# Kernel optimization log

Hardware: AMD Instinct MI355X
Metric: run time of the kernel (lower is better)

Reference implementation:

```python
import jax, jax.numpy as jnp
import numpy as np

D_MODEL = 1024
HEADDIM = 64
EXPAND = 2
D_STATE = 128
D_CONV = 4
NGROUPS = 1
D_INNER = EXPAND * D_MODEL            # 2048
NHEADS = D_INNER // HEADDIM           # 32
CONV_DIM = D_INNER + 2 * NGROUPS * D_STATE
D_IN_PROJ = 2 * D_INNER + 2 * NGROUPS * D_STATE + NHEADS
BATCH = 2
SEQLEN = 1024
EPS = 1e-5


def silu(v):
    return v * jax.nn.sigmoid(v)


def setup_inputs() -> dict:
    key = jax.random.key(0)
    ks = jax.random.split(key, 8)
    s = 0.02
    return {
        "x": jax.random.normal(ks[0], (BATCH, SEQLEN, D_MODEL), jnp.float32),
        "in_proj_w": jax.random.normal(ks[1], (D_IN_PROJ, D_MODEL), jnp.float32) * s,
        "conv_w": jax.random.normal(ks[2], (CONV_DIM, D_CONV), jnp.float32) * 0.2,
        "conv_b": jax.random.normal(ks[3], (CONV_DIM,), jnp.float32) * 0.02,
        "dt_bias": jax.random.normal(ks[4], (NHEADS,), jnp.float32) * 0.1,
        "A_log": jax.random.normal(ks[5], (NHEADS,), jnp.float32) * 0.5,
        "D": jax.random.normal(ks[6], (NHEADS,), jnp.float32) * 0.5,
        "norm_w": jnp.ones((D_INNER,), jnp.float32),
        "out_proj_w": jax.random.normal(ks[7], (D_MODEL, D_INNER), jnp.float32) * s,
    }


def _mamba2(x, in_proj_w, conv_w, conv_b, dt_bias, A_log, D, norm_w, out_proj_w):
    b, l, _ = x.shape
    # input projection -> z | xBC | dt
    zxbcdt = x @ in_proj_w.T                                  # [b,l,d_in_proj]
    z, xBC, dt = jnp.split(zxbcdt, [D_INNER, D_INNER + CONV_DIM], axis=-1)
    dt = jax.nn.softplus(dt + dt_bias)                        # [b,l,nh]
    # causal depthwise conv over time, then SiLU
    rhs = conv_w.T[:, None, :]                                # [d_conv, 1, conv_dim]
    xBC = jax.lax.conv_general_dilated(
        xBC, rhs, window_strides=(1,), padding=[(D_CONV - 1, 0)],
        dimension_numbers=("NWC", "WIO", "NWC"), feature_group_count=CONV_DIM)
    xBC = silu(xBC + conv_b)
    xs, Bm, Cm = jnp.split(xBC, [D_INNER, D_INNER + D_STATE], axis=-1)
    xs = xs.reshape(b, l, NHEADS, HEADDIM)                    # [b,l,h,p]
    A = -jnp.exp(A_log)                                       # [nh], negative
    dA = jnp.exp(dt * A)                                      # [b,l,nh] in (0,1)
    # selective scan: h_t = dA_t * h_{t-1} + dt_t * x_t (outer) B_t; y_t = h_t C_t
    def step(h, inp):
        dA_t, x_t, B_t, dt_t, C_t = inp                       # [b,h],[b,h,p],[b,n],[b,h],[b,n]
        h = h * dA_t[:, :, None, None] + jnp.einsum("bh,bhp,bn->bhpn", dt_t, x_t, B_t)
        y = jnp.einsum("bhpn,bn->bhp", h, C_t)
        return h, y

    h0 = jnp.zeros((b, NHEADS, HEADDIM, D_STATE), x.dtype)
    xs_t = xs.transpose(1, 0, 2, 3)
    _, ys = jax.lax.scan(step, h0, (dA.transpose(1, 0, 2), xs_t,
                                    Bm.transpose(1, 0, 2), dt.transpose(1, 0, 2),
                                    Cm.transpose(1, 0, 2)))
    y = ys.transpose(1, 0, 2, 3) + D[None, None, :, None] * xs  # skip term
    y = y.reshape(b, l, D_INNER)
    # gated RMSNorm (norm_before_gate=False): rmsnorm(y * silu(z)) * w
    y = y * silu(z)
    y = y * jax.lax.rsqrt(jnp.mean(y * y, axis=-1, keepdims=True) + EPS) * norm_w
    return y @ out_proj_w.T


def reference(x, in_proj_w, conv_w, conv_b, dt_bias, A_log, D, norm_w, out_proj_w):
    return x + _mamba2(x, in_proj_w, conv_w, conv_b, dt_bias, A_log, D, norm_w, out_proj_w)
```

## Files before the change

### kernel.cpp

```cpp
#include <hip/hip_runtime.h>
#include <hip/hip_bf16.h>
#include <math.h>

#define NHEADS   32
#define CONV_DIM 2304
#define D_INNER  2048
#define SEQLEN   1024
#define NROWS    2048
#define ZX_STR   4352
#define D_MODEL  1024
#define Q        64
#define NCHUNK   16
#define XT_STR   72

typedef __attribute__((ext_vector_type(8))) short bhalf8;
typedef __attribute__((ext_vector_type(8))) short short8;
typedef __attribute__((ext_vector_type(4))) short short4v;
typedef __attribute__((ext_vector_type(4))) float f32x4;

__device__ __forceinline__ float bf2f(__hip_bfloat16 v){ return __bfloat162float(v); }
__device__ __forceinline__ short f2bs(float f){ __hip_bfloat16 h = __float2bfloat16(f); return *(short*)&h; }
__device__ __forceinline__ float s2f(short s){ __hip_bfloat16 h = *(__hip_bfloat16*)&s; return __bfloat162float(h); }
__device__ __forceinline__ float rdin(const void* p, size_t i, int isf){
    return isf ? ((const float*)p)[i] : __bfloat162float(((const __hip_bfloat16*)p)[i]);
}

#define XN8 262144
#define WN8 561152
#define ON8 262144
__global__ __launch_bounds__(256)
void to_bf16_all(const void* __restrict__ xs, const void* __restrict__ ws,
                 const void* __restrict__ os, const void* __restrict__ normw,
                 __hip_bfloat16* __restrict__ xd, __hip_bfloat16* __restrict__ wd,
                 __hip_bfloat16* __restrict__ od, int* __restrict__ flagp)
{
    const unsigned short* xu = (const unsigned short*)xs;
    int cnt = 0;
    for (int k = threadIdx.x; k < 4096; k += 256) {
        int e = (xu[2 * k] >> 7) & 0xFF;
        cnt += (e >= 90 && e <= 141) ? 1 : 0;
    }
#pragma unroll
    for (int m = 1; m < 64; m <<= 1) cnt += __shfl_xor(cnt, m);
    __shared__ int red[4];
    if ((threadIdx.x & 63) == 0) red[threadIdx.x >> 6] = cnt;
    __syncthreads();
    const int isf = ((red[0] + red[1] + red[2] + red[3]) < 2048) ? 1 : 0;
    if (blockIdx.x == 0 && threadIdx.x == 0) *flagp = isf;

    int i = blockIdx.x * 256 + threadIdx.x;
    if (i < XN8 + WN8) {
        const void* src; __hip_bfloat16* dst; int j;
        if (i < XN8) { src = xs; dst = xd; j = i; }
        else         { src = ws; dst = wd; j = i - XN8; }
        if (isf) {
            const float4* s = (const float4*)src;
            float4 a = s[2 * j], b = s[2 * j + 1];
            short8 r;
            r[0]=f2bs(a.x); r[1]=f2bs(a.y); r[2]=f2bs(a.z); r[3]=f2bs(a.w);
            r[4]=f2bs(b.x); r[5]=f2bs(b.y); r[6]=f2bs(b.z); r[7]=f2bs(b.w);
            ((short8*)dst)[j] = r;
        } else {
            ((float4*)dst)[j] = ((const float4*)src)[j];
        }
    } else {
        int j = i - XN8 - WN8;
        int k0 = (j * 8) & (D_INNER - 1);
        float v[8];
        if (isf) {
            const float4* s = (const float4*)os;
            float4 a = s[2 * j], b = s[2 * j + 1];
            v[0]=a.x; v[1]=a.y; v[2]=a.z; v[3]=a.w;
            v[4]=b.x; v[5]=b.y; v[6]=b.z; v[7]=b.w;
        } else {
            bhalf8 a = ((const bhalf8*)os)[j];
#pragma unroll
            for (int q = 0; q < 8; ++q) v[q] = s2f(a[q]);
        }
        short8 r;
#pragma unroll
        for (int q = 0; q < 8; ++q)
            r[q] = f2bs(v[q] * rdin(normw, k0 + q, isf));
        ((short8*)od)[j] = r;
    }
}

template<int MODE, int MT, int NT, int WROWS, int WCOLS>
__global__ __launch_bounds__(256)
void gemm_bt(const __hip_bfloat16* __restrict__ A,
             const __hip_bfloat16* __restrict__ W,
             __hip_bfloat16* __restrict__ Cb,
             const void* __restrict__ xraw,
             void* __restrict__ outv,
             const float* __restrict__ rowsum,
             const int* __restrict__ flagp,
             int K, int N)
{
    constexpr int FM = MT / WROWS / 16;
    constexpr int FN = NT / WCOLS / 16;
    constexpr int AI = MT / 32;
    constexpr int BI = NT / 32;
    __shared__ short As[MT * 64];
    __shared__ short Bs[NT * 64];
    const int m0 = blockIdx.y * MT;
    const int n0 = blockIdx.x * NT;
    const int wave = threadIdx.x >> 6;
    const int lane = threadIdx.x & 63;
    const int lr8 = lane >> 3, lc8 = lane & 7;
    const int lr  = lane & 15, lq  = lane >> 4;
    const int wm = (wave / WCOLS) * (MT / WROWS);
    const int wn = (wave % WCOLS) * (NT / WCOLS);
    const int swl = lr & 7;

    f32x4 acc[FM][FN];
#pragma unroll
    for (int i = 0; i < FM; ++i)
#pragma unroll
        for (int j = 0; j < FN; ++j) acc[i][j] = (f32x4){0.f,0.f,0.f,0.f};

    for (int k0 = 0; k0 < K; k0 += 64) {
#pragma unroll
        for (int i = 0; i < AI; ++i) {
            const int rt = (wave * AI + i) * 8;
            const __hip_bfloat16* gp = A + (size_t)(m0 + rt + lr8) * K + k0 + ((lc8 ^ lr8) << 3);
            __builtin_amdgcn_global_load_lds(
                (const __attribute__((address_space(1))) void*)gp,
                (__attribute__((address_space(3))) void*)&As[rt * 64], 16, 0, 0);
        }
#pragma unroll
        for (int i = 0; i < BI; ++i) {
            const int rt = (wave * BI + i) * 8;
            const __hip_bfloat16* gp = W + (size_t)(n0 + rt + lr8) * K + k0 + ((lc8 ^ lr8) << 3);
            __builtin_amdgcn_global_load_lds(
                (const __attribute__((address_space(1))) void*)gp,
                (__attribute__((address_space(3))) void*)&Bs[rt * 64], 16, 0, 0);
        }
        __syncthreads();
#pragma unroll
        for (int kk = 0; kk < 64; kk += 32) {
            const int sw = (((kk >> 3) + lq) ^ swl) << 3;
            bhalf8 af[FM], bfv[FN];
#pragma unroll
            for (int t = 0; t < FM; ++t)
                af[t]  = *(const bhalf8*)&As[(wm + t * 16 + lr) * 64 + sw];
#pragma unroll
            for (int t = 0; t < FN; ++t)
                bfv[t] = *(const bhalf8*)&Bs[(wn + t * 16 + lr) * 64 + sw];
#pragma unroll
            for (int ti = 0; ti < FM; ++ti)
#pragma unroll
                for (int tj = 0; tj < FN; ++tj)
                    acc[ti][tj] = __builtin_amdgcn_mfma_f32_16x16x32_bf16(
                        af[ti], bfv[tj], acc[ti][tj], 0, 0, 0);
        }
        __syncthreads();
    }

    const int isf = (MODE == 1) ? *flagp : 0;
#pragma unroll
    for (int ti = 0; ti < FM; ++ti)
#pragma unroll
        for (int tj = 0; tj < FN; ++tj)
#pragma unroll
            for (int r = 0; r < 4; ++r) {
                int m = m0 + wm + ti * 16 + lq * 4 + r;
                int n = n0 + wn + tj * 16 + lr;
                size_t idx = (size_t)m * N + n;
                float v = acc[ti][tj][r];
                if (MODE == 0) {
                    Cb[idx] = __float2bfloat16(v);
                } else {
                    float scale = rsqrtf(rowsum[m] / (float)D_INNER + 1e-5f);
                    v = v * scale + rdin(xraw, idx, isf);
                    if (isf) ((float*)outv)[idx] = v;
                    else     ((__hip_bfloat16*)outv)[idx] = __float2bfloat16(v);
                }
            }
}

__global__ __launch_bounds__(256)
void convdt(const __hip_bfloat16* __restrict__ zxb,
            const void* __restrict__ conv_w, const void* __restrict__ conv_b,
            const void* __restrict__ xraw, const void* __restrict__ wraw,
            const void* __restrict__ dt_bias,
            const int* __restrict__ flagp,
            __hip_bfloat16* __restrict__ xs_bf,
            __hip_bfloat16* __restrict__ B_bf,
            __hip_bfloat16* __restrict__ C_bf,
            float* __restrict__ dtp)
{
    __shared__ short smem[11 * CONV_DIM];
    const int isf = *flagp;

    if (blockIdx.x < 256) {
        const int r0 = blockIdx.x * 8;
        const int bstart = r0 & ~(SEQLEN - 1);
        for (int idx = threadIdx.x; idx < 11 * (CONV_DIM / 8); idx += 256) {
            int ii = idx / (CONV_DIM / 8);
            int seg = idx % (CONV_DIM / 8);
            int g = r0 - 3 + ii;
            bhalf8 v;
            if (g >= bstart) {
                v = *(const bhalf8*)&zxb[(size_t)g * ZX_STR + 2048 + seg * 8];
            } else {
#pragma unroll
                for (int j = 0; j < 8; ++j) v[j] = 0;
            }
            *(bhalf8*)&smem[ii * CONV_DIM + seg * 8] = v;
        }
        __syncthreads();

#pragma unroll
        for (int sIt = 0; sIt < 2; ++sIt) {
            const int seg = threadIdx.x + sIt * 256;
            if (seg >= CONV_DIM / 8) break;
            const int c0 = seg * 8;
            float wt[8][4], bias[8];
            if (isf) {
                const float4* wp = (const float4*)conv_w;
#pragma unroll
                for (int u = 0; u < 8; ++u) {
                    float4 q = wp[c0 + u];
                    wt[u][0]=q.x; wt[u][1]=q.y; wt[u][2]=q.z; wt[u][3]=q.w;
                }
                float4 b0 = ((const float4*)conv_b)[seg * 2];
                float4 b1 = ((const float4*)conv_b)[seg * 2 + 1];
                bias[0]=b0.x; bias[1]=b0.y; bias[2]=b0.z; bias[3]=b0.w;
                bias[4]=b1.x; bias[5]=b1.y; bias[6]=b1.z; bias[7]=b1.w;
            } else {
                const bhalf8* wp = (const bhalf8*)conv_w;
#pragma unroll
                for (int u = 0; u < 4; ++u) {
                    bhalf8 q = wp[seg * 4 + u];
#pragma unroll
                    for (int t4 = 0; t4 < 4; ++t4) {
                        wt[2*u][t4]   = s2f(q[t4]);
                        wt[2*u+1][t4] = s2f(q[4 + t4]);
                    }
                }
                bhalf8 bq = ((const bhalf8*)conv_b)[seg];
#pragma unroll
                for (int j = 0; j < 8; ++j) bias[j] = s2f(bq[j]);
            }
#pragma unroll
            for (int r = 0; r < 8; ++r) {
                bhalf8 i0 = *(const bhalf8*)&smem[(r + 0) * CONV_DIM + c0];
                bhalf8 i1 = *(const bhalf8*)&smem[(r + 1) * CONV_DIM + c0];
                bhalf8 i2 = *(const bhalf8*)&smem[(r + 2) * CONV_DIM + c0];
                bhalf8 i3 = *(const bhalf8*)&smem[(r + 3) * CONV_DIM + c0];
                bhalf8 out;
#pragma unroll
                for (int j = 0; j < 8; ++j) {
                    float acc = bias[j];
                    acc = fmaf(s2f(i0[j]), wt[j][0], acc);
                    acc = fmaf(s2f(i1[j]), wt[j][1], acc);
                    acc = fmaf(s2f(i2[j]), wt[j][2], acc);
                    acc = fmaf(s2f(i3[j]), wt[j][3], acc);
                    out[j] = f2bs(acc / (1.f + expf(-acc)));
                }
                const int row = r0 + r;
                if (c0 < 2048)
                    *(bhalf8*)&xs_bf[(size_t)row * 2048 + c0] = out;
                else if (c0 < 2176)
                    *(bhalf8*)&B_bf[(size_t)row * 128 + (c0 - 2048)] = out;
                else
                    *(bhalf8*)&C_bf[(size_t)row * 128 + (c0 - 2176)] = out;
            }
        }
    } else {
        float* xsh = (float*)smem;
        const int r0 = (blockIdx.x - 256) * 8;
        if (isf) {
            const float4* xp = (const float4*)xraw;
            for (int i4 = threadIdx.x; i4 < 2048; i4 += 256)
                *(float4*)&xsh[i4 * 4] = xp[(size_t)r0 * 256 + i4];
        } else {
            const bhalf8* xp = (const bhalf8*)xraw;
            for (int i8 = threadIdx.x; i8 < 1024; i8 += 256) {
                bhalf8 v = xp[(size_t)r0 * 128 + i8];
#pragma unroll
                for (int q = 0; q < 8; ++q) xsh[i8 * 8 + q] = s2f(v[q]);
            }
        }
        __syncthreads();
        const int h = threadIdx.x >> 3;
        const int t = threadIdx.x & 7;
        const size_t wb = (size_t)(4352 + h) * D_MODEL;
        float s[8];
#pragma unroll
        for (int r = 0; r < 8; ++r) s[r] = 0.f;
        if (isf) {
            const float4* wp = (const float4*)wraw;
            for (int k0 = 0; k0 < D_MODEL; k0 += 32) {
                float4 w4 = wp[(wb + k0) / 4 + t];
#pragma unroll
                for (int r = 0; r < 8; ++r) {
                    float4 x4 = *(const float4*)&xsh[r * D_MODEL + k0 + t * 4];
                    s[r] = fmaf(w4.x, x4.x, fmaf(w4.y, x4.y,
                           fmaf(w4.z, x4.z, fmaf(w4.w, x4.w, s[r]))));
                }
            }
        } else {
            const __hip_bfloat16* wp = (const __hip_bfloat16*)wraw;
            for (int k0 = 0; k0 < D_MODEL; k0 += 64) {
                bhalf8 w8 = *(const bhalf8*)&wp[wb + k0 + t * 8];
#pragma unroll
                for (int r = 0; r < 8; ++r) {
                    float4 xa = *(const float4*)&xsh[r * D_MODEL + k0 + t * 8];
                    float4 xb = *(const float4*)&xsh[r * D_MODEL + k0 + t * 8 + 4];
                    s[r] = fmaf(s2f(w8[0]), xa.x, fmaf(s2f(w8[1]), xa.y,
                           fmaf(s2f(w8[2]), xa.z, fmaf(s2f(w8[3]), xa.w, s[r]))));
                    s[r] = fmaf(s2f(w8[4]), xb.x, fmaf(s2f(w8[5]), xb.y,
                           fmaf(s2f(w8[6]), xb.z, fmaf(s2f(w8[7]), xb.w, s[r]))));
                }
            }
        }
#pragma unroll
        for (int r = 0; r < 8; ++r) {
            s[r] += __shfl_xor(s[r], 1);
            s[r] += __shfl_xor(s[r], 2);
            s[r] += __shfl_xor(s[r], 4);
        }
        if (t == 0) {
            float bias = rdin(dt_bias, h, isf);
#pragma unroll
            for (int r = 0; r < 8; ++r) {
                float raw = s[r] + bias;
                dtp[(size_t)(r0 + r) * NHEADS + h] = raw > 20.f ? raw : log1pf(expf(raw));
            }
        }
    }
}

__global__ __launch_bounds__(256)
void chunk_kernel(const __hip_bfloat16* __restrict__ xs_bf,
                  const __hip_bfloat16* __restrict__ B_bf,
                  const float* __restrict__ dtp, const void* __restrict__ Alog,
                  const int* __restrict__ flagp,
                  float* __restrict__ cumg, float* __restrict__ decayg,
                  __hip_bfloat16* __restrict__ Sb,
                  float* __restrict__ rowsum)
{
    __shared__ float cumS[Q], uS[Q];
    __shared__ short Xt[64 * XT_STR];
    __shared__ short Bt[128 * XT_STR];
    const int bhc = blockIdx.x;
    const int c = bhc & 15, h = (bhc >> 4) & 31, b = bhc >> 9;
    const int row0 = b * SEQLEN + c * Q;
    const int isf = *flagp;

    if (threadIdx.x < 2) rowsum[bhc * 2 + threadIdx.x] = 0.f;
    if (threadIdx.x < 64) {
        const int t = threadIdx.x;
        const float An = -expf(rdin(Alog, h, isf));
        const float dt = dtp[(size_t)(row0 + t) * NHEADS + h];
        float cum = dt * An;
#pragma unroll
        for (int ofs = 1; ofs < 64; ofs <<= 1) {
            float v = __shfl_up(cum, ofs);
            if (t >= ofs) cum += v;
        }
        float tot = __shfl(cum, 63);
        cumS[t] = cum;
        uS[t] = expf(tot - cum) * dt;
        cumg[(size_t)bhc * Q + t] = cum;
        if (t == 63) decayg[bhc] = expf(tot);
    }
    __syncthreads();

#pragma unroll
    for (int i = 0; i < 2; ++i) {
        int seg = threadIdx.x + i * 256;
        int t = seg >> 3, p8 = (seg & 7) * 8;
        float ut = uS[t];
        bhalf8 v = *(const bhalf8*)&xs_bf[(size_t)(row0 + t) * 2048 + h * 64 + p8];
#pragma unroll
        for (int j = 0; j < 8; ++j)
            Xt[(p8 + j) * XT_STR + t] = f2bs(s2f(v[j]) * ut);
    }
#pragma unroll
    for (int i = 0; i < 4; ++i) {
        int seg = threadIdx.x + i * 256;
        int t = seg >> 4, n8 = (seg & 15) * 8;
        bhalf8 v = *(const bhalf8*)&B_bf[(size_t)(row0 + t) * 128 + n8];
#pragma unroll
        for (int j = 0; j < 8; ++j)
            Bt[(n8 + j) * XT_STR + t] = v[j];
    }
    __syncthreads();

    const int wave = threadIdx.x >> 6, lane = threadIdx.x & 63;
    const int lr = lane & 15, lq = lane >> 4;
    const int p0 = wave * 16;
    f32x4 acc[8];
#pragma unroll
    for (int j = 0; j < 8; ++j) acc[j] = (f32x4){0.f,0.f,0.f,0.f};
#pragma unroll
    for (int kk = 0; kk < 64; kk += 32) {
        bhalf8 af = *(const bhalf8*)&Xt[(p0 + lr) * XT_STR + kk + lq * 8];
#pragma unroll
        for (int j = 0; j < 8; ++j) {
            bhalf8 bf = *(const bhalf8*)&Bt[(j * 16 + lr) * XT_STR + kk + lq * 8];
            acc[j] = __builtin_amdgcn_mfma_f32_16x16x32_bf16(af, bf, acc[j], 0, 0, 0);
        }
    }
#pragma unroll
    for (int j = 0; j < 8; ++j)
#pragma unroll
        for (int r = 0; r < 4; ++r) {
            int p = p0 + lq * 4 + r;
            int n = j * 16 + lr;
            Sb[(size_t)bhc * 8192 + p * 128 + n] = __float2bfloat16(acc[j][r]);
        }
}

__global__ __launch_bounds__(256)
void rec_kernel(const __hip_bfloat16* __restrict__ Sb,
                const float* __restrict__ decayg,
                __hip_bfloat16* __restrict__ hst)
{
    const int bh = blockIdx.x >> 3;
    const int sl = blockIdx.x & 7;
    const int off = sl * 1024 + threadIdx.x * 4;
    float h0 = 0.f, h1 = 0.f, h2 = 0.f, h3 = 0.f;
    for (int c = 0; c < NCHUNK; ++c) {
        size_t base = ((size_t)bh * NCHUNK + c) * 8192 + off;
        short4v hb;
        hb[0] = f2bs(h0); hb[1] = f2bs(h1); hb[2] = f2bs(h2); hb[3] = f2bs(h3);
        *(short4v*)&hst[base] = hb;
        short4v sv = *(const short4v*)&Sb[base];
        float d = decayg[bh * NCHUNK + c];
        h0 = fmaf(h0, d, s2f(sv[0])); h1 = fmaf(h1, d, s2f(sv[1]));
        h2 = fmaf(h2, d, s2f(sv[2])); h3 = fmaf(h3, d, s2f(sv[3]));
    }
}

__global__ __launch_bounds__(256)
void y_kernel(const __hip_bfloat16* __restrict__ xs_bf,
              const __hip_bfloat16* __restrict__ B_bf,
              const __hip_bfloat16* __restrict__ C_bf,
              const __hip_bfloat16* __restrict__ hst,
              const float* __restrict__ cumg,
              const float* __restrict__ dtp,
              const __hip_bfloat16* __restrict__ zxb,
              const void* __restrict__ Draw, const int* __restrict__ flagp,
              __hip_bfloat16* __restrict__ vbuf, float* __restrict__ rowsum)
{
    __shared__ short Xt[64 * XT_STR];
    __shared__ short zS[64 * XT_STR];
    __shared__ short Mt[64 * XT_STR];
    __shared__ float cumS[Q], dtS[Q];
    const int bhc = blockIdx.x;
    const int c = bhc & 15, h = (bhc >> 4) & 31, b = bhc >> 9;
    const int row0 = b * SEQLEN + c * Q;
    const int isf = *flagp;
    const float Dh = rdin(Draw, h, isf);

    if (threadIdx.x < 64) {
        cumS[threadIdx.x] = cumg[(size_t)bhc * Q + threadIdx.x];
        dtS[threadIdx.x]  = dtp[(size_t)(row0 + threadIdx.x) * NHEADS + h];
    }
#pragma unroll
    for (int i = 0; i < 2; ++i) {
        int seg = threadIdx.x + i * 256;
        int t = seg >> 3, p8 = (seg & 7) * 8;
        bhalf8 v = *(const bhalf8*)&xs_bf[(size_t)(row0 + t) * 2048 + h * 64 + p8];
#pragma unroll
        for (int j = 0; j < 8; ++j)
            Xt[(p8 + j) * XT_STR + t] = v[j];
        bhalf8 zv = *(const bhalf8*)&zxb[(size_t)(row0 + t) * ZX_STR + h * 64 + p8];
        *(bhalf8*)&zS[t * XT_STR + p8] = zv;
    }
    __syncthreads();

    const int wave = threadIdx.x >> 6, lane = threadIdx.x & 63;
    const int lr = lane & 15, lq = lane >> 4;
    const int t0 = wave * 16;

    {
        f32x4 accg[4];
#pragma unroll
        for (int j = 0; j < 4; ++j) accg[j] = (f32x4){0.f,0.f,0.f,0.f};
#pragma unroll
        for (int kk = 0; kk < 128; kk += 32) {
            bhalf8 af = *(const bhalf8*)&C_bf[(size_t)(row0 + t0 + lr) * 128 + kk + lq * 8];
#pragma unroll
            for (int j = 0; j < 4; ++j) {
                bhalf8 bf = *(const bhalf8*)&B_bf[(size_t)(row0 + j * 16 + lr) * 128 + kk + lq * 8];
                accg[j] = __builtin_amdgcn_mfma_f32_16x16x32_bf16(af, bf, accg[j], 0, 0, 0);
            }
        }
#pragma unroll
        for (int j = 0; j < 4; ++j)
#pragma unroll
            for (int r = 0; r < 4; ++r) {
                int t = t0 + lq * 4 + r;
                int s = j * 16 + lr;
                float m = (s <= t) ? accg[j][r] * expf(cumS[t] - cumS[s]) * dtS[s] : 0.f;
                Mt[t * XT_STR + s] = f2bs(m);
            }
    }
    __syncthreads();

    f32x4 acc1[4], acc2[4];
#pragma unroll
    for (int j = 0; j < 4; ++j) { acc1[j] = (f32x4){0.f,0.f,0.f,0.f}; acc2[j] = acc1[j]; }
#pragma unroll
    for (int kk = 0; kk < 64; kk += 32) {
        bhalf8 af = *(const bhalf8*)&Mt[(t0 + lr) * XT_STR + kk + lq * 8];
#pragma unroll
        for (int j = 0; j < 4; ++j) {
            bhalf8 bf = *(const bhalf8*)&Xt[(j * 16 + lr) * XT_STR + kk + lq * 8];
            acc1[j] = __builtin_amdgcn_mfma_f32_16x16x32_bf16(af, bf, acc1[j], 0, 0, 0);
        }
    }
#pragma unroll
    for (int kk = 0; kk < 128; kk += 32) {
        bhalf8 af = *(const bhalf8*)&C_bf[(size_t)(row0 + t0 + lr) * 128 + kk + lq * 8];
#pragma unroll
        for (int j = 0; j < 4; ++j) {
            bhalf8 bf = *(const bhalf8*)&hst[(size_t)bhc * 8192 + (j * 16 + lr) * 128 + kk + lq * 8];
            acc2[j] = __builtin_amdgcn_mfma_f32_16x16x32_bf16(af, bf, acc2[j], 0, 0, 0);
        }
    }
    float ex[4];
#pragma unroll
    for (int r = 0; r < 4; ++r) ex[r] = expf(cumS[t0 + lq * 4 + r]);

    float vv[4][4];
    float s2[4] = {0.f, 0.f, 0.f, 0.f};
#pragma unroll
    for (int j = 0; j < 4; ++j)
#pragma unroll
        for (int r = 0; r < 4; ++r) {
            int t = t0 + lq * 4 + r;
            int p = j * 16 + lr;
            float xv = s2f(Xt[p * XT_STR + t]);
            float y = acc1[j][r] + ex[r] * acc2[j][r] + Dh * xv;
            float zz = s2f(zS[t * XT_STR + p]);
            float v = y * (zz / (1.f + expf(-zz)));
            vv[j][r] = v;
            s2[r] += v * v;
        }
#pragma unroll
    for (int r = 0; r < 4; ++r) {
        s2[r] += __shfl_xor(s2[r], 1);
        s2[r] += __shfl_xor(s2[r], 2);
        s2[r] += __shfl_xor(s2[r], 4);
        s2[r] += __shfl_xor(s2[r], 8);
    }
    if (lr == 0)
#pragma unroll
        for (int r = 0; r < 4; ++r)
            atomicAdd(&rowsum[row0 + t0 + lq * 4 + r], s2[r]);

    __syncthreads();
#pragma unroll
    for (int j = 0; j < 4; ++j)
#pragma unroll
        for (int r = 0; r < 4; ++r)
            zS[(t0 + lq * 4 + r) * XT_STR + j * 16 + lr] = f2bs(vv[j][r]);
    __syncthreads();
#pragma unroll
    for (int i = 0; i < 2; ++i) {
        int seg = threadIdx.x + i * 256;
        int t = seg >> 3, p8 = (seg & 7) * 8;
        bhalf8 o = *(const bhalf8*)&zS[t * XT_STR + p8];
        *(bhalf8*)&vbuf[(size_t)(row0 + t) * D_INNER + h * 64 + p8] = o;
    }
}

extern "C" void kernel_launch(void* const* d_in, const int* in_sizes, int n_in,
                              void* d_out, int out_size, void* d_ws, size_t ws_size,
                              hipStream_t stream)
{
    const void* x_raw    = d_in[0];
    const void* inw_raw  = d_in[1];
    const void* convw    = d_in[2];
    const void* convb    = d_in[3];
    const void* dtb      = d_in[4];
    const void* Alog     = d_in[5];
    const void* Dsk      = d_in[6];
    const void* normw    = d_in[7];
    const void* outw_raw = d_in[8];

    char* ws = (char*)d_ws;
    size_t off = 0;
    int* flag = (int*)(ws + off);                      off += 256;
    float* rowsum = (float*)(ws + off);                off += (size_t)NROWS * 4;
    __hip_bfloat16* xb    = (__hip_bfloat16*)(ws+off); off += (size_t)NROWS * D_MODEL * 2;
    __hip_bfloat16* inwb  = (__hip_bfloat16*)(ws+off); off += (size_t)4384 * D_MODEL * 2;
    __hip_bfloat16* outwb = (__hip_bfloat16*)(ws+off); off += (size_t)D_MODEL * D_INNER * 2;
    __hip_bfloat16* zxb   = (__hip_bfloat16*)(ws+off); off += (size_t)NROWS * ZX_STR * 2;
    __hip_bfloat16* xs_bf = (__hip_bfloat16*)(ws+off); off += (size_t)NROWS * 2048 * 2;
    __hip_bfloat16* B_bf  = (__hip_bfloat16*)(ws+off); off += (size_t)NROWS * 128 * 2;
    __hip_bfloat16* C_bf  = (__hip_bfloat16*)(ws+off); off += (size_t)NROWS * 128 * 2;
    float* dtp   = (float*)(ws+off);                   off += (size_t)NROWS * NHEADS * 4;
    float* cumg  = (float*)(ws+off);                   off += (size_t)1024 * Q * 4;
    float* decayg= (float*)(ws+off);                   off += (size_t)1024 * 4;
    __hip_bfloat16* hst   = (__hip_bfloat16*)(ws+off); off += (size_t)1024 * 8192 * 2;
    __hip_bfloat16* Sb    = (__hip_bfloat16*)(ws+off); off += (size_t)1024 * 8192 * 2;
    __hip_bfloat16* vbuf = Sb;

    to_bf16_all<<<(XN8+WN8+ON8)/256, 256, 0, stream>>>(x_raw, inw_raw, outw_raw,
                                                       normw, xb, inwb, outwb, flag);
    gemm_bt<0,64,128,1,4><<<dim3(34, 32), 256, 0, stream>>>(
        xb, inwb, zxb, nullptr, nullptr, nullptr, flag, D_MODEL, ZX_STR);
    convdt<<<512, 256, 0, stream>>>(zxb, convw, convb, x_raw, inw_raw, dtb, flag,
                                    xs_bf, B_bf, C_bf, dtp);
    chunk_kernel<<<1024, 256, 0, stream>>>(xs_bf, B_bf, dtp, Alog, flag,
                                           cumg, decayg, Sb, rowsum);
    rec_kernel<<<512, 256, 0, stream>>>(Sb, decayg, hst);
    y_kernel<<<1024, 256, 0, stream>>>(xs_bf, B_bf, C_bf, hst, cumg, dtp, zxb,
                                       Dsk, flag, vbuf, rowsum);
    gemm_bt<1,64,64,2,2><<<dim3(16, 32), 256, 0, stream>>>(
        vbuf, outwb, nullptr, x_raw, d_out, rowsum, flag, D_INNER, D_MODEL);
}
```

Before: 225.2 us.

## Fuse chunk, recurrence and output scan stages into one cooperative kernel

The separate chunk, inter-chunk recurrence and y/gating kernels are replaced by one cooperative kernel. Its three phases are separated by grid-wide syncs, and the X tile and per-chunk cumulative decays stay in shared memory across phases. B is pre-scaled by the decay-weighted dt before the chunk-state MFMA, and the y phase reads C and B straight from global memory. This removes two kernel boundaries and some global round trips. In exchange it requires all 1024 blocks to be co-resident, adds grid-sync cost, and keeps the old three-kernel path as a fallback when occupancy is too low.

```diff
diff --git a/kernel.cpp b/kernel.cpp
--- a/kernel.cpp
+++ b/kernel.cpp
@@ -1,6 +1,9 @@
 #include <hip/hip_runtime.h>
 #include <hip/hip_bf16.h>
+#include <hip/hip_cooperative_groups.h>
 #include <math.h>
+
+namespace cg = cooperative_groups;
 
 #define NHEADS   32
 #define CONV_DIM 2304
@@ -15,6 +18,7 @@
 
 typedef __attribute__((ext_vector_type(8))) short bhalf8;
 typedef __attribute__((ext_vector_type(8))) short short8;
+typedef __attribute__((ext_vector_type(2))) short short2v;
 typedef __attribute__((ext_vector_type(4))) short short4v;
 typedef __attribute__((ext_vector_type(4))) float f32x4;
 
@@ -332,6 +336,223 @@
     }
 }
 
+__global__ __launch_bounds__(256, 4)
+void scan_fused(const __hip_bfloat16* __restrict__ xs_bf,
+                const __hip_bfloat16* __restrict__ B_bf,
+                const __hip_bfloat16* __restrict__ C_bf,
+                const float* __restrict__ dtp, const void* __restrict__ Alog,
+                const int* __restrict__ flagp,
+                float* __restrict__ decayg,
+                __hip_bfloat16* __restrict__ Sb,
+                __hip_bfloat16* __restrict__ hst,
+                const __hip_bfloat16* __restrict__ zxb,
+                const void* __restrict__ Draw,
+                __hip_bfloat16* __restrict__ vbuf,
+                float* __restrict__ rowsum)
+{
+    __shared__ short Xt[64 * XT_STR];
+    __shared__ short BtU[128 * XT_STR];
+    __shared__ float cumS[Q], uS[Q], dtS[Q];
+    const int bhc = blockIdx.x;
+    const int c = bhc & 15, h = (bhc >> 4) & 31, b = bhc >> 9;
+    const int row0 = b * SEQLEN + c * Q;
+    const int isf = *flagp;
+    const int wave = threadIdx.x >> 6, lane = threadIdx.x & 63;
+    const int lr = lane & 15, lq = lane >> 4;
+
+    if (threadIdx.x < 2) rowsum[bhc * 2 + threadIdx.x] = 0.f;
+
+    if (threadIdx.x < 64) {
+        const int t = threadIdx.x;
+        const float An = -expf(rdin(Alog, h, isf));
+        const float dt = dtp[(size_t)(row0 + t) * NHEADS + h];
+        float cum = dt * An;
+#pragma unroll
+        for (int ofs = 1; ofs < 64; ofs <<= 1) {
+            float v = __shfl_up(cum, ofs);
+            if (t >= ofs) cum += v;
+        }
+        float tot = __shfl(cum, 63);
+        cumS[t] = cum; dtS[t] = dt;
+        uS[t] = expf(tot - cum) * dt;
+        if (t == 63) decayg[bhc] = expf(tot);
+    }
+    __syncthreads();
+
+#pragma unroll
+    for (int i = 0; i < 2; ++i) {
+        int seg = threadIdx.x + i * 256;
+        int t = seg >> 3, p8 = (seg & 7) * 8;
+        bhalf8 v = *(const bhalf8*)&xs_bf[(size_t)(row0 + t) * 2048 + h * 64 + p8];
+#pragma unroll
+        for (int j = 0; j < 8; ++j)
+            Xt[(p8 + j) * XT_STR + t] = v[j];
+    }
+#pragma unroll
+    for (int i = 0; i < 4; ++i) {
+        int seg = threadIdx.x + i * 256;
+        int t = seg >> 4, n8 = (seg & 15) * 8;
+        float ut = uS[t];
+        bhalf8 v = *(const bhalf8*)&B_bf[(size_t)(row0 + t) * 128 + n8];
+#pragma unroll
+        for (int j = 0; j < 8; ++j)
+            BtU[(n8 + j) * XT_STR + t] = f2bs(s2f(v[j]) * ut);
+    }
+    __syncthreads();
+
+    {
+        const int p0 = wave * 16;
+        f32x4 acc[8];
+#pragma unroll
+        for (int j = 0; j < 8; ++j) acc[j] = (f32x4){0.f,0.f,0.f,0.f};
+#pragma unroll
+        for (int kk = 0; kk < 64; kk += 32) {
+            bhalf8 af = *(const bhalf8*)&Xt[(p0 + lr) * XT_STR + kk + lq * 8];
+#pragma unroll
+            for (int j = 0; j < 8; ++j) {
+                bhalf8 bf = *(const bhalf8*)&BtU[(j * 16 + lr) * XT_STR + kk + lq * 8];
+                acc[j] = __builtin_amdgcn_mfma_f32_16x16x32_bf16(af, bf, acc[j], 0, 0, 0);
+            }
+        }
+#pragma unroll
+        for (int j = 0; j < 8; ++j)
+#pragma unroll
+            for (int r = 0; r < 4; ++r) {
+                int p = p0 + lq * 4 + r;
+                int n = j * 16 + lr;
+                Sb[(size_t)bhc * 8192 + p * 128 + n] = __float2bfloat16(acc[j][r]);
+            }
+    }
+    __threadfence();
+    cg::this_grid().sync();
+    __threadfence();
+
+    {
+        const int bh = blockIdx.x >> 4;
+        const int sl = blockIdx.x & 15;
+        const int off = sl * 512 + threadIdx.x * 2;
+        float h0 = 0.f, h1 = 0.f;
+        for (int cc = 0; cc < NCHUNK; ++cc) {
+            size_t base = ((size_t)bh * NCHUNK + cc) * 8192 + off;
+            short2v hb;
+            hb[0] = f2bs(h0); hb[1] = f2bs(h1);
+            *(short2v*)&hst[base] = hb;
+            short2v sv = *(const short2v*)&Sb[base];
+            float d = decayg[bh * NCHUNK + cc];
+            h0 = fmaf(h0, d, s2f(sv[0]));
+            h1 = fmaf(h1, d, s2f(sv[1]));
+        }
+    }
+    __threadfence();
+    cg::this_grid().sync();
+    __threadfence();
+
+    short* zS = BtU;
+    short* Mt = BtU + 64 * XT_STR;
+    const float Dh = rdin(Draw, h, isf);
+
+#pragma unroll
+    for (int i = 0; i < 2; ++i) {
+        int seg = threadIdx.x + i * 256;
+        int t = seg >> 3, p8 = (seg & 7) * 8;
+        bhalf8 zv = *(const bhalf8*)&zxb[(size_t)(row0 + t) * ZX_STR + h * 64 + p8];
+        *(bhalf8*)&zS[t * XT_STR + p8] = zv;
+    }
+
+    const int t0 = wave * 16;
+    {
+        f32x4 accg[4];
+#pragma unroll
+        for (int j = 0; j < 4; ++j) accg[j] = (f32x4){0.f,0.f,0.f,0.f};
+#pragma unroll
+        for (int kk = 0; kk < 128; kk += 32) {
+            bhalf8 af = *(const bhalf8*)&C_bf[(size_t)(row0 + t0 + lr) * 128 + kk + lq * 8];
+#pragma unroll
+            for (int j = 0; j < 4; ++j) {
+                bhalf8 bf = *(const bhalf8*)&B_bf[(size_t)(row0 + j * 16 + lr) * 128 + kk + lq * 8];
+                accg[j] = __builtin_amdgcn_mfma_f32_16x16x32_bf16(af, bf, accg[j], 0, 0, 0);
+            }
+        }
+#pragma unroll
+        for (int j = 0; j < 4; ++j)
+#pragma unroll
+            for (int r = 0; r < 4; ++r) {
+                int t = t0 + lq * 4 + r;
+                int s = j * 16 + lr;
+                float m = (s <= t) ? accg[j][r] * expf(cumS[t] - cumS[s]) * dtS[s] : 0.f;
+                Mt[t * XT_STR + s] = f2bs(m);
+            }
+    }
+    __syncthreads();
+
+    f32x4 acc1[4], acc2[4];
+#pragma unroll
+    for (int j = 0; j < 4; ++j) { acc1[j] = (f32x4){0.f,0.f,0.f,0.f}; acc2[j] = acc1[j]; }
+#pragma unroll
+    for (int kk = 0; kk < 64; kk += 32) {
+        bhalf8 af = *(const bhalf8*)&Mt[(t0 + lr) * XT_STR + kk + lq * 8];
+#pragma unroll
+        for (int j = 0; j < 4; ++j) {
+            bhalf8 bf = *(const bhalf8*)&Xt[(j * 16 + lr) * XT_STR + kk + lq * 8];
+            acc1[j] = __builtin_amdgcn_mfma_f32_16x16x32_bf16(af, bf, acc1[j], 0, 0, 0);
+        }
+    }
+#pragma unroll
+    for (int kk = 0; kk < 128; kk += 32) {
+        bhalf8 af = *(const bhalf8*)&C_bf[(size_t)(row0 + t0 + lr) * 128 + kk + lq * 8];
+#pragma unroll
+        for (int j = 0; j < 4; ++j) {
+            bhalf8 bf = *(const bhalf8*)&hst[(size_t)bhc * 8192 + (j * 16 + lr) * 128 + kk + lq * 8];
+            acc2[j] = __builtin_amdgcn_mfma_f32_16x16x32_bf16(af, bf, acc2[j], 0, 0, 0);
+        }
+    }
+    float ex[4];
+#pragma unroll
+    for (int r = 0; r < 4; ++r) ex[r] = expf(cumS[t0 + lq * 4 + r]);
+
+    float vv[4][4];
+    float s2[4] = {0.f, 0.f, 0.f, 0.f};
+#pragma unroll
+    for (int j = 0; j < 4; ++j)
+#pragma unroll
+        for (int r = 0; r < 4; ++r) {
+            int t = t0 + lq * 4 + r;
+            int p = j * 16 + lr;
+            float xv = s2f(Xt[p * XT_STR + t]);
+            float y = acc1[j][r] + ex[r] * acc2[j][r] + Dh * xv;
+            float zz = s2f(zS[t * XT_STR + p]);
+            float v = y * (zz / (1.f + expf(-zz)));
+            vv[j][r] = v;
+            s2[r] += v * v;
+        }
+#pragma unroll
+    for (int r = 0; r < 4; ++r) {
+        s2[r] += __shfl_xor(s2[r], 1);
+        s2[r] += __shfl_xor(s2[r], 2);
+        s2[r] += __shfl_xor(s2[r], 4);
+        s2[r] += __shfl_xor(s2[r], 8);
+    }
+    if (lr == 0)
+#pragma unroll
+        for (int r = 0; r < 4; ++r)
+            atomicAdd(&rowsum[row0 + t0 + lq * 4 + r], s2[r]);
+
+    __syncthreads();
+#pragma unroll
+    for (int j = 0; j < 4; ++j)
+#pragma unroll
+        for (int r = 0; r < 4; ++r)
+            zS[(t0 + lq * 4 + r) * XT_STR + j * 16 + lr] = f2bs(vv[j][r]);
+    __syncthreads();
+#pragma unroll
+    for (int i = 0; i < 2; ++i) {
+        int seg = threadIdx.x + i * 256;
+        int t = seg >> 3, p8 = (seg & 7) * 8;
+        bhalf8 o = *(const bhalf8*)&zS[t * XT_STR + p8];
+        *(bhalf8*)&vbuf[(size_t)(row0 + t) * D_INNER + h * 64 + p8] = o;
+    }
+}
+
 __global__ __launch_bounds__(256)
 void chunk_kernel(const __hip_bfloat16* __restrict__ xs_bf,
                   const __hip_bfloat16* __restrict__ B_bf,
@@ -608,11 +829,25 @@
         xb, inwb, zxb, nullptr, nullptr, nullptr, flag, D_MODEL, ZX_STR);
     convdt<<<512, 256, 0, stream>>>(zxb, convw, convb, x_raw, inw_raw, dtb, flag,
                                     xs_bf, B_bf, C_bf, dtp);
-    chunk_kernel<<<1024, 256, 0, stream>>>(xs_bf, B_bf, dtp, Alog, flag,
-                                           cumg, decayg, Sb, rowsum);
-    rec_kernel<<<512, 256, 0, stream>>>(Sb, decayg, hst);
-    y_kernel<<<1024, 256, 0, stream>>>(xs_bf, B_bf, C_bf, hst, cumg, dtp, zxb,
-                                       Dsk, flag, vbuf, rowsum);
+
+    int maxb = 0;
+    hipError_t qe = hipOccupancyMaxActiveBlocksPerMultiprocessor(&maxb, scan_fused, 256, 0);
+    if (qe == hipSuccess && maxb >= 4) {
+        void* args[] = {
+            (void*)&xs_bf, (void*)&B_bf, (void*)&C_bf, (void*)&dtp,
+            (void*)&Alog, (void*)&flag, (void*)&decayg, (void*)&Sb,
+            (void*)&hst, (void*)&zxb, (void*)&Dsk, (void*)&vbuf, (void*)&rowsum
+        };
+        hipLaunchCooperativeKernel((void*)scan_fused, dim3(1024), dim3(256),
+                                   args, 0, stream);
+    } else {
+        chunk_kernel<<<1024, 256, 0, stream>>>(xs_bf, B_bf, dtp, Alog, flag,
+                                               cumg, decayg, Sb, rowsum);
+        rec_kernel<<<512, 256, 0, stream>>>(Sb, decayg, hst);
+        y_kernel<<<1024, 256, 0, stream>>>(xs_bf, B_bf, C_bf, hst, cumg, dtp, zxb,
+                                           Dsk, flag, vbuf, rowsum);
+    }
+
     gemm_bt<1,64,64,2,2><<<dim3(16, 32), 256, 0, stream>>>(
         vbuf, outwb, nullptr, x_raw, d_out, rowsum, flag, D_INNER, D_MODEL);
 }
```

New measurement: 226.6 us. No clear change (+0.6%).
